# Kernel tuning notes

Hardware: AMD Instinct MI355X
Metric: run time of the kernel (lower is better)

The kernel has to match this reference:

```python
import jax, jax.numpy as jnp
import numpy as np

N = 100000          # nodes
E = 1600000         # edges (avg degree 16)
F_IN = 128          # input node features
H1, C1 = 8, 8       # conv1: 8 heads, 8 channels/head -> 64 concat
NUM_CLASSES = 40    # conv2: 1 head, 40 channels
EPS = 1e-16         # PyG softmax denominator epsilon
NEG_SLOPE = 0.2     # PyG GATConv default leaky_relu slope


def setup_inputs() -> dict:
    key = jax.random.key(0)
    ks = jax.random.split(key, 12)
    x = jax.random.normal(ks[0], (N, F_IN), jnp.float32)
    edge_index = jax.random.randint(ks[1], (2, E), 0, N, dtype=jnp.int64)
    edge_attr = jax.random.normal(ks[2], (E, 1), jnp.float32)
    # layer 1 params (Glorot-ish scaling)
    s1 = 1.0 / np.sqrt(F_IN)
    W1 = jax.random.normal(ks[3], (F_IN, H1 * C1), jnp.float32) * s1
    a_src1 = jax.random.normal(ks[4], (H1, C1), jnp.float32) * (1.0 / np.sqrt(C1))
    a_dst1 = jax.random.normal(ks[5], (H1, C1), jnp.float32) * (1.0 / np.sqrt(C1))
    b1 = jnp.zeros((H1 * C1,), jnp.float32)
    # layer 2 params: in = 64 (conv1 concat output), 1 head, NUM_CLASSES channels
    s2 = 1.0 / np.sqrt(H1 * C1)
    W2 = jax.random.normal(ks[6], (H1 * C1, NUM_CLASSES), jnp.float32) * s2
    a_src2 = jax.random.normal(ks[7], (1, NUM_CLASSES), jnp.float32) * (1.0 / np.sqrt(NUM_CLASSES))
    a_dst2 = jax.random.normal(ks[8], (1, NUM_CLASSES), jnp.float32) * (1.0 / np.sqrt(NUM_CLASSES))
    b2 = jnp.zeros((NUM_CLASSES,), jnp.float32)
    return {"x": x, "edge_index": edge_index, "edge_attr": edge_attr,
            "W1": W1, "a_src1": a_src1, "a_dst1": a_dst1, "b1": b1,
            "W2": W2, "a_src2": a_src2, "a_dst2": a_dst2, "b2": b2}


def gat_conv(x, src, dst, W, a_s, a_d, b, heads, out_ch):
    """PyG GATConv: linear -> per-edge leaky-relu attention -> dst softmax -> scatter-add."""
    n = x.shape[0]
    h = (x @ W).reshape(n, heads, out_ch)                 # [N,H,C]
    alpha_s = jnp.sum(h * a_s, axis=-1)                   # [N,H]
    alpha_d = jnp.sum(h * a_d, axis=-1)                   # [N,H]
    e = jax.nn.leaky_relu(alpha_s[src] + alpha_d[dst], NEG_SLOPE)  # [Etot,H]
    # segment softmax over incoming edges per destination node
    m = jax.ops.segment_max(e, dst, num_segments=n)       # [N,H]
    e = jnp.exp(e - m[dst])
    denom = jax.ops.segment_sum(e, dst, num_segments=n)   # [N,H]
    alpha = e / (denom[dst] + EPS)                        # [Etot,H]
    msg = h[src] * alpha[:, :, None]                      # [Etot,H,C]
    out = jax.ops.segment_sum(msg, dst, num_segments=n)   # [N,H,C]
    return out.reshape(n, heads * out_ch) + b             # concat heads + bias


def reference(x, edge_index, edge_attr, W1, a_src1, a_dst1, b1, W2, a_src2, a_dst2, b2):
    n = x.shape[0]
    # PyG GATConv adds self-loops by default
    loops = jnp.arange(n, dtype=edge_index.dtype)
    src = jnp.concatenate([edge_index[0], loops])
    dst = jnp.concatenate([edge_index[1], loops])
    x = x.astype(jnp.float32)
    x1 = jax.nn.elu(gat_conv(x, src, dst, W1, a_src1, a_dst1, b1, H1, C1))
    x2 = jax.nn.elu(gat_conv(x1, src, dst, W2, a_src2, a_dst2, b2, 1, NUM_CLASSES))
    return x2
```

## Files before the change

kernel.cpp:

```cpp
#include <hip/hip_runtime.h>
#include <math.h>

#define NN 100000
#define NE 1600000
#define NETOT (NE + NN)
#define FIN 128
#define H1N 8
#define D1 64
#define NC 40
#define LNT 64
#define LOG2E 1.44269504088896f

#define BSH 9
#define BNODES 512
#define NBUC ((NN + BNODES - 1) / BNODES)
#define EPB 4096
#define NBLKA ((NE + EPB - 1) / EPB)
#define BCAP 9216
#define LB ((NN + LNT - 1) / LNT)

__device__ __forceinline__ float leakyf(float x) { return x >= 0.0f ? x : 0.2f * x; }
__device__ __forceinline__ float eluf(float x)   { return x > 0.0f ? x : expm1f(x); }
__device__ __forceinline__ float exp2fast(float x) { return __builtin_amdgcn_exp2f(x); }

__device__ __forceinline__ unsigned short f2bf(float f) {
  unsigned u = __float_as_uint(f);
  u += 0x7fffu + ((u >> 16) & 1u);
  return (unsigned short)(u >> 16);
}
__device__ __forceinline__ float bflo(unsigned u) { return __uint_as_float(u << 16); }
__device__ __forceinline__ float bfhi(unsigned u) { return __uint_as_float(u & 0xffff0000u); }

__global__ void k_detect(const long long* __restrict__ ei, int* __restrict__ flag,
                         int* __restrict__ bcnt) {
  int t = threadIdx.x;
  if (t < NBUC) bcnt[t] = 0;
  if (t == 0) {
    int is64 = 1;
    for (int i = 0; i < 16; ++i) {
      long long v = ei[i];
      if (v < 0 || v >= NN) is64 = 0;
    }
    *flag = is64;
  }
}

#define XS1(node, k) xs[(node) * FIN + ((k) ^ ((node) & 31))]
__global__ __launch_bounds__(512) void k_fusedA(
    const void* __restrict__ ei, const int* __restrict__ flag,
    unsigned int* __restrict__ subbuf, int* __restrict__ bcnt,
    const float* __restrict__ x, const float* __restrict__ W,
    const float* __restrict__ aw_s, const float* __restrict__ aw_d,
    unsigned short* __restrict__ h, float* __restrict__ als,
    float* __restrict__ ald) {
  __shared__ __align__(16) char smem[65536];
  int t = threadIdx.x;
  if (blockIdx.x < NBLKA) {
    unsigned int*   pay    = (unsigned int*)smem;
    unsigned int*   spay   = pay + EPB;
    unsigned short* bk     = (unsigned short*)(spay + EPB);
    unsigned short* sbk    = bk + EPB;
    int*            hist   = (int*)(sbk + EPB);
    int*            lstart = hist + 256;
    int*            cur    = lstart + 256;
    int*            gbase  = cur + 256;
    int e0 = blockIdx.x * EPB;
    int cnt = min(EPB, NE - e0);
    if (t < 256) hist[t] = 0;
    __syncthreads();
    bool f64 = (*flag) != 0;
    for (int i = t; i < cnt; i += 512) {
      int s, d;
      if (f64) {
        const long long* p = (const long long*)ei;
        s = (int)p[e0 + i]; d = (int)p[NE + e0 + i];
      } else {
        const int* p = (const int*)ei;
        s = p[e0 + i]; d = p[NE + e0 + i];
      }
      int b = d >> BSH;
      pay[i] = ((unsigned)s << BSH) | (unsigned)(d & (BNODES - 1));
      bk[i] = (unsigned short)b;
      atomicAdd(&hist[b], 1);
    }
    __syncthreads();
    int v = 0;
    if (t < 256) { v = hist[t]; lstart[t] = v; }
    __syncthreads();
    for (int st = 1; st < 256; st <<= 1) {
      int xv = (t < 256 && t >= st) ? lstart[t - st] : 0;
      __syncthreads();
      if (t < 256) lstart[t] += xv;
      __syncthreads();
    }
    int excl = 0;
    if (t < 256) excl = lstart[t] - v;
    __syncthreads();
    if (t < 256) {
      lstart[t] = excl;
      cur[t] = excl;
      gbase[t] = (v > 0) ? atomicAdd(&bcnt[t], v) : 0;
    }
    __syncthreads();
    for (int i = t; i < cnt; i += 512) {
      int b = bk[i];
      int pos = atomicAdd(&cur[b], 1);
      spay[pos] = pay[i];
      sbk[pos] = (unsigned short)b;
    }
    __syncthreads();
    for (int i = t; i < cnt; i += 512) {
      int b = sbk[i];
      int o = gbase[b] + (i - lstart[b]);
      if (o < BCAP) subbuf[(size_t)b * BCAP + o] = spay[i];
    }
  } else {
    float* ws = (float*)smem;
    float* xs = ws + FIN * D1;
    int base = (blockIdx.x - NBLKA) * LNT;
    for (int i = t; i < FIN * D1; i += 512) ws[i] = W[i];
    for (int i = t; i < LNT * FIN; i += 512) {
      int node = i >> 7, k = i & 127;
      int gn = base + node;
      if (gn >= NN) gn = NN - 1;
      XS1(node, k) = x[(size_t)gn * FIN + k];
    }
    __syncthreads();
    int g = t & 7, nl = t >> 3;
    float acc[8] = {0, 0, 0, 0, 0, 0, 0, 0};
    #pragma unroll 4
    for (int k = 0; k < FIN; ++k) {
      float x0 = XS1(nl, k);
      const float4* wr = (const float4*)&ws[k * D1 + g * 8];
      float4 wa = wr[0], wb = wr[1];
      acc[0] = fmaf(x0, wa.x, acc[0]);
      acc[1] = fmaf(x0, wa.y, acc[1]);
      acc[2] = fmaf(x0, wa.z, acc[2]);
      acc[3] = fmaf(x0, wa.w, acc[3]);
      acc[4] = fmaf(x0, wb.x, acc[4]);
      acc[5] = fmaf(x0, wb.y, acc[5]);
      acc[6] = fmaf(x0, wb.z, acc[6]);
      acc[7] = fmaf(x0, wb.w, acc[7]);
    }
    int n0 = base + nl;
    if (n0 < NN) {
      float s = 0.f, d = 0.f;
      uint4 pk;
      pk.x = (unsigned)f2bf(acc[0]) | ((unsigned)f2bf(acc[1]) << 16);
      pk.y = (unsigned)f2bf(acc[2]) | ((unsigned)f2bf(acc[3]) << 16);
      pk.z = (unsigned)f2bf(acc[4]) | ((unsigned)f2bf(acc[5]) << 16);
      pk.w = (unsigned)f2bf(acc[6]) | ((unsigned)f2bf(acc[7]) << 16);
      *(uint4*)(void*)(h + (size_t)n0 * D1 + g * 8) = pk;
      #pragma unroll
      for (int c = 0; c < 8; ++c) {
        s = fmaf(acc[c], aw_s[g * 8 + c], s);
        d = fmaf(acc[c], aw_d[g * 8 + c], d);
      }
      als[n0 * H1N + g] = s * LOG2E;
      ald[n0 * H1N + g] = d * LOG2E;
    }
  }
}

__global__ __launch_bounds__(256) void k_passB(const int* __restrict__ bcnt,
                       const unsigned int* __restrict__ subbuf,
                       int* __restrict__ row_start, int* __restrict__ csr) {
  __shared__ int hist[BNODES];
  __shared__ int ps[256];
  __shared__ int cur[BNODES];
  __shared__ int bbs;
  int b = blockIdx.x, t = threadIdx.x;
  int d0 = b << BSH;
  int nloc = min(BNODES, NN - d0);
  int tot = 0;
  if (t < NBUC) {
    int dd = t << BSH;
    tot = min(BNODES, NN - dd) + min(bcnt[t], BCAP);
  }
  ps[t] = tot;
  __syncthreads();
  for (int s = 1; s < 256; s <<= 1) {
    int xv = (t >= s) ? ps[t - s] : 0;
    __syncthreads();
    ps[t] += xv;
    __syncthreads();
  }
  if (t == 0) bbs = (b == 0) ? 0 : ps[b - 1];
  if (b == 0 && t == 0) row_start[NN] = ps[NBUC - 1];
  __syncthreads();
  int bucket_base = bbs;
  hist[t] = 0; hist[t + 256] = 0;
  __syncthreads();
  int cnt = min(bcnt[b], BCAP);
  const unsigned int* sb = subbuf + (size_t)b * BCAP;
  for (int i = t; i < cnt; i += 256)
    atomicAdd(&hist[sb[i] & (BNODES - 1)], 1);
  __syncthreads();
  int j0 = 2 * t, j1 = 2 * t + 1;
  int s0 = (j0 < nloc) ? hist[j0] + 1 : 0;
  int s1 = (j1 < nloc) ? hist[j1] + 1 : 0;
  int pairsum = s0 + s1;
  ps[t] = pairsum;
  __syncthreads();
  for (int s = 1; s < 256; s <<= 1) {
    int x = (t >= s) ? ps[t - s] : 0;
    __syncthreads();
    ps[t] += x;
    __syncthreads();
  }
  int excl = ps[t] - pairsum + bucket_base;
  if (j0 < nloc) {
    row_start[d0 + j0] = excl;
    csr[excl] = d0 + j0;
    cur[j0] = excl + 1;
  }
  if (j1 < nloc) {
    int rs = excl + s0;
    row_start[d0 + j1] = rs;
    csr[rs] = d0 + j1;
    cur[j1] = rs + 1;
  }
  __syncthreads();
  for (int i = t; i < cnt; i += 256) {
    unsigned u = sb[i];
    int pos = atomicAdd(&cur[u & (BNODES - 1)], 1);
    csr[pos] = (int)(u >> BSH);
  }
}

#define XS2(node, k) xs[(node) * D1 + ((k) ^ ((node) & 31))]
__global__ __launch_bounds__(512) void k_lin2(
    const unsigned int* __restrict__ x1bf, const float* __restrict__ W,
    const float* __restrict__ aw_s, const float* __restrict__ aw_d,
    unsigned short* __restrict__ h, float* __restrict__ als,
    float* __restrict__ ald) {
  __shared__ float ws[D1 * D1];
  __shared__ float xs[LNT * D1];
  int t = threadIdx.x;
  int base = blockIdx.x * LNT;
  for (int i = t; i < D1 * D1; i += 512) {
    int k = i >> 6, c = i & 63;
    ws[i] = (c < NC) ? W[k * NC + c] : 0.f;
  }
  for (int i = t; i < LNT * 32; i += 512) {
    int node = i >> 5, kd = i & 31;
    int gn = base + node;
    if (gn >= NN) gn = NN - 1;
    unsigned u = x1bf[(size_t)gn * 32 + kd];
    XS2(node, 2 * kd)     = bflo(u);
    XS2(node, 2 * kd + 1) = bfhi(u);
  }
  __syncthreads();
  int g = t & 7, nl = t >> 3;
  float acc[8] = {0, 0, 0, 0, 0, 0, 0, 0};
  #pragma unroll 4
  for (int k = 0; k < D1; ++k) {
    float x0 = XS2(nl, k);
    const float4* wr = (const float4*)&ws[k * D1 + g * 8];
    float4 wa = wr[0], wb = wr[1];
    acc[0] = fmaf(x0, wa.x, acc[0]);
    acc[1] = fmaf(x0, wa.y, acc[1]);
    acc[2] = fmaf(x0, wa.z, acc[2]);
    acc[3] = fmaf(x0, wa.w, acc[3]);
    acc[4] = fmaf(x0, wb.x, acc[4]);
    acc[5] = fmaf(x0, wb.y, acc[5]);
    acc[6] = fmaf(x0, wb.z, acc[6]);
    acc[7] = fmaf(x0, wb.w, acc[7]);
  }
  int n0 = base + nl;
  float s = 0.f, d = 0.f;
  #pragma unroll
  for (int c = 0; c < 8; ++c) {
    int col = g * 8 + c;
    float aws = (col < NC) ? aw_s[col] : 0.f;
    float awd = (col < NC) ? aw_d[col] : 0.f;
    s = fmaf(acc[c], aws, s);
    d = fmaf(acc[c], awd, d);
  }
  s += __shfl_xor(s, 1); d += __shfl_xor(d, 1);
  s += __shfl_xor(s, 2); d += __shfl_xor(d, 2);
  s += __shfl_xor(s, 4); d += __shfl_xor(d, 4);
  if (n0 < NN) {
    if (g < 5) {
      #pragma unroll
      for (int c = 0; c < 8; ++c) h[(size_t)n0 * NC + g * 8 + c] = f2bf(acc[c]);
    }
    if (g == 0) { als[n0] = s * LOG2E; ald[n0] = d * LOG2E; }
  }
}

__global__ void k_node1(const int* __restrict__ row_start, const int* __restrict__ csr,
                        const unsigned short* __restrict__ h, const float* __restrict__ als,
                        const float* __restrict__ ald, const float* __restrict__ b,
                        unsigned int* __restrict__ x1bf) {
  __shared__ float pl[4][2][32 * 9];
  int wid = threadIdx.x >> 6, half = (threadIdx.x >> 5) & 1, c2 = threadIdx.x & 31;
  int n = blockIdx.x * 8 + wid * 2 + half;
  float* pw = pl[wid][half];
  const unsigned int* h32 = (const unsigned int*)h;
  int r0 = row_start[n], r1 = row_start[n + 1];
  int hd = c2 >> 2;
  const float4* adp = (const float4*)(ald + (size_t)n * H1N);
  float4 ad0 = adp[0], ad1 = adp[1];
  float S = 0.f;
  float alo0 = 0.f, ahi0 = 0.f, alo1 = 0.f, ahi1 = 0.f;
  float alo2 = 0.f, ahi2 = 0.f, alo3 = 0.f, ahi3 = 0.f;
  for (int kb = r0; kb < r1; kb += 32) {
    int cnt = min(32, r1 - kb);
    if (c2 < cnt) {
      int sk = csr[kb + c2];
      const float4* ap = (const float4*)(als + (size_t)sk * H1N);
      float4 a0 = ap[0], a1 = ap[1];
      pw[c2 * 9 + 0] = exp2fast(leakyf(a0.x + ad0.x));
      pw[c2 * 9 + 1] = exp2fast(leakyf(a0.y + ad0.y));
      pw[c2 * 9 + 2] = exp2fast(leakyf(a0.z + ad0.z));
      pw[c2 * 9 + 3] = exp2fast(leakyf(a0.w + ad0.w));
      pw[c2 * 9 + 4] = exp2fast(leakyf(a1.x + ad1.x));
      pw[c2 * 9 + 5] = exp2fast(leakyf(a1.y + ad1.y));
      pw[c2 * 9 + 6] = exp2fast(leakyf(a1.z + ad1.z));
      pw[c2 * 9 + 7] = exp2fast(leakyf(a1.w + ad1.w));
      pw[c2 * 9 + 8] = __int_as_float(sk);
    }
    asm volatile("s_waitcnt lgkmcnt(0)" ::: "memory");
    int j = 0;
    for (; j + 4 <= cnt; j += 4) {
      int s0 = __float_as_int(pw[(j + 0) * 9 + 8]);
      int s1 = __float_as_int(pw[(j + 1) * 9 + 8]);
      int s2 = __float_as_int(pw[(j + 2) * 9 + 8]);
      int s3 = __float_as_int(pw[(j + 3) * 9 + 8]);
      float p0 = pw[(j + 0) * 9 + hd], p1 = pw[(j + 1) * 9 + hd];
      float p2 = pw[(j + 2) * 9 + hd], p3 = pw[(j + 3) * 9 + hd];
      unsigned u0 = h32[(unsigned)s0 * 32 + c2];
      unsigned u1 = h32[(unsigned)s1 * 32 + c2];
      unsigned u2 = h32[(unsigned)s2 * 32 + c2];
      unsigned u3 = h32[(unsigned)s3 * 32 + c2];
      alo0 = fmaf(p0, bflo(u0), alo0); ahi0 = fmaf(p0, bfhi(u0), ahi0);
      alo1 = fmaf(p1, bflo(u1), alo1); ahi1 = fmaf(p1, bfhi(u1), ahi1);
      alo2 = fmaf(p2, bflo(u2), alo2); ahi2 = fmaf(p2, bfhi(u2), ahi2);
      alo3 = fmaf(p3, bflo(u3), alo3); ahi3 = fmaf(p3, bfhi(u3), ahi3);
      S += (p0 + p1) + (p2 + p3);
    }
    for (; j < cnt; ++j) {
      int s0 = __float_as_int(pw[j * 9 + 8]);
      float p0 = pw[j * 9 + hd];
      unsigned u0 = h32[(unsigned)s0 * 32 + c2];
      alo0 = fmaf(p0, bflo(u0), alo0); ahi0 = fmaf(p0, bfhi(u0), ahi0);
      S += p0;
    }
  }
  float alo = (alo0 + alo1) + (alo2 + alo3);
  float ahi = (ahi0 + ahi1) + (ahi2 + ahi3);
  float inv = 1.0f / (S + 1e-16f);
  float ox = eluf(alo * inv + b[2 * c2 + 0]);
  float oy = eluf(ahi * inv + b[2 * c2 + 1]);
  x1bf[(size_t)n * 32 + c2] = (unsigned)f2bf(ox) | ((unsigned)f2bf(oy) << 16);
}

__global__ void k_node2(const int* __restrict__ row_start, const int* __restrict__ csr,
                        const unsigned short* __restrict__ h, const float* __restrict__ als,
                        const float* __restrict__ ald, const float* __restrict__ b,
                        float* __restrict__ out) {
  __shared__ float pl[4][3][20 * 2];
  int wid = threadIdx.x >> 6, lane = threadIdx.x & 63;
  int g = lane / 20, q = lane - g * 20;
  int gg = g < 3 ? g : 2;
  int n = blockIdx.x * 12 + wid * 3 + gg;
  bool live = (g < 3) && (n < NN);
  if (n >= NN) n = NN - 1;
  float* pw = pl[wid][gg];
  const unsigned int* h32 = (const unsigned int*)h;
  int r0 = row_start[n], r1 = row_start[n + 1];
  float aldn = ald[n];
  float S = 0.f;
  float alo0 = 0.f, ahi0 = 0.f, alo1 = 0.f, ahi1 = 0.f;
  float alo2 = 0.f, ahi2 = 0.f, alo3 = 0.f, ahi3 = 0.f;
  for (int kb = r0; kb < r1; kb += 20) {
    int cnt = min(20, r1 - kb);
    if (q < cnt && g < 3) {
      int sk = csr[kb + q];
      pw[q * 2 + 0] = exp2fast(leakyf(als[sk] + aldn));
      pw[q * 2 + 1] = __int_as_float(sk);
    }
    asm volatile("s_waitcnt lgkmcnt(0)" ::: "memory");
    int j = 0;
    for (; j + 4 <= cnt; j += 4) {
      int s0 = __float_as_int(pw[(j + 0) * 2 + 1]);
      int s1 = __float_as_int(pw[(j + 1) * 2 + 1]);
      int s2 = __float_as_int(pw[(j + 2) * 2 + 1]);
      int s3 = __float_as_int(pw[(j + 3) * 2 + 1]);
      float p0 = pw[(j + 0) * 2], p1 = pw[(j + 1) * 2];
      float p2 = pw[(j + 2) * 2], p3 = pw[(j + 3) * 2];
      unsigned u0 = h32[(unsigned)s0 * 20 + q];
      unsigned u1 = h32[(unsigned)s1 * 20 + q];
      unsigned u2 = h32[(unsigned)s2 * 20 + q];
      unsigned u3 = h32[(unsigned)s3 * 20 + q];
      alo0 = fmaf(p0, bflo(u0), alo0); ahi0 = fmaf(p0, bfhi(u0), ahi0);
      alo1 = fmaf(p1, bflo(u1), alo1); ahi1 = fmaf(p1, bfhi(u1), ahi1);
      alo2 = fmaf(p2, bflo(u2), alo2); ahi2 = fmaf(p2, bfhi(u2), ahi2);
      alo3 = fmaf(p3, bflo(u3), alo3); ahi3 = fmaf(p3, bfhi(u3), ahi3);
      S += (p0 + p1) + (p2 + p3);
    }
    for (; j < cnt; ++j) {
      int s0 = __float_as_int(pw[j * 2 + 1]);
      float p0 = pw[j * 2];
      unsigned u0 = h32[(unsigned)s0 * 20 + q];
      alo0 = fmaf(p0, bflo(u0), alo0); ahi0 = fmaf(p0, bfhi(u0), ahi0);
      S += p0;
    }
  }
  float alo = (alo0 + alo1) + (alo2 + alo3);
  float ahi = (ahi0 + ahi1) + (ahi2 + ahi3);
  if (live) {
    float inv = 1.0f / (S + 1e-16f);
    float2 o;
    o.x = eluf(alo * inv + b[2 * q + 0]);
    o.y = eluf(ahi * inv + b[2 * q + 1]);
    ((float2*)out)[(size_t)n * 20 + q] = o;
  }
}

extern "C" void kernel_launch(void* const* d_in, const int* in_sizes, int n_in,
                              void* d_out, int out_size, void* d_ws, size_t ws_size,
                              hipStream_t stream) {
  const float* x    = (const float*)d_in[0];
  const void*  ei   = d_in[1];
  const float* W1   = (const float*)d_in[3];
  const float* as1w = (const float*)d_in[4];
  const float* ad1w = (const float*)d_in[5];
  const float* b1   = (const float*)d_in[6];
  const float* W2   = (const float*)d_in[7];
  const float* as2w = (const float*)d_in[8];
  const float* ad2w = (const float*)d_in[9];
  const float* b2   = (const float*)d_in[10];
  float* out = (float*)d_out;

  char* w = (char*)d_ws;
  size_t off = 0;
  auto carve = [&](size_t bytes) -> void* {
    void* r = w + off;
    off += (bytes + 255) & ~(size_t)255;
    return r;
  };
  int*            flag        = (int*)carve(256);
  int*            bcnt        = (int*)carve((size_t)NBUC * 4);
  unsigned int*   subbuf      = (unsigned int*)carve((size_t)NBUC * BCAP * 4);
  int*            row_start   = (int*)carve((size_t)(NN + 1) * 4);
  int*            csr         = (int*)carve((size_t)NETOT * 4);
  unsigned short* h1          = (unsigned short*)carve((size_t)NN * D1 * 2);
  float*          als1        = (float*)carve((size_t)NN * H1N * 4);
  float*          ald1        = (float*)carve((size_t)NN * H1N * 4);
  unsigned int*   x1bf        = (unsigned int*)carve((size_t)NN * 32 * 4);
  unsigned short* h2 = h1; float* als2 = als1; float* ald2 = ald1;

  k_detect<<<1, 256, 0, stream>>>((const long long*)ei, flag, bcnt);

  k_fusedA<<<NBLKA + LB, 512, 0, stream>>>(ei, flag, subbuf, bcnt,
                                           x, W1, as1w, ad1w, h1, als1, ald1);

  k_passB<<<NBUC, 256, 0, stream>>>(bcnt, subbuf, row_start, csr);

  k_node1<<<NN / 8, 256, 0, stream>>>(row_start, csr, h1, als1, ald1, b1, x1bf);

  k_lin2<<<LB, 512, 0, stream>>>(x1bf, W2, as2w, ad2w, h2, als2, ald2);
  k_node2<<<(NN + 11) / 12, 256, 0, stream>>>(row_start, csr, h2, als2, ald2, b2, out);
}
```

Before: 203.8 us.

## Fuse layer-2 linear projection and attention logits into layer-1 aggregation kernel

Removes the separate k_lin2 kernel by having each half-wave in the layer-1 node aggregation kernel compute its node's 64x40 projection directly from the ELU output kept in shared memory, with W2 staged per block as packed bf16. This avoids writing and re-reading the x1 intermediate (100k x 64 bf16) and saves one launch. In exchange every block reloads and converts W2 into LDS, W2 is now held in bf16 rather than fp32, and the aggregation kernel uses more shared memory and registers, which may lower occupancy.

```diff
diff --git a/kernel.cpp b/kernel.cpp
--- a/kernel.cpp
+++ b/kernel.cpp
@@ -228,75 +228,29 @@
   }
 }
 
-#define XS2(node, k) xs[(node) * D1 + ((k) ^ ((node) & 31))]
-__global__ __launch_bounds__(512) void k_lin2(
-    const unsigned int* __restrict__ x1bf, const float* __restrict__ W,
-    const float* __restrict__ aw_s, const float* __restrict__ aw_d,
-    unsigned short* __restrict__ h, float* __restrict__ als,
-    float* __restrict__ ald) {
-  __shared__ float ws[D1 * D1];
-  __shared__ float xs[LNT * D1];
+__global__ __launch_bounds__(256) void k_node1f(
+    const int* __restrict__ row_start, const int* __restrict__ csr,
+    const unsigned short* __restrict__ h, const float* __restrict__ als,
+    const float* __restrict__ ald, const float* __restrict__ b,
+    const float* __restrict__ W2, const float* __restrict__ aw_s2,
+    const float* __restrict__ aw_d2, unsigned int* __restrict__ h2_32,
+    float* __restrict__ als2, float* __restrict__ ald2) {
+  __shared__ float pl[4][2][32 * 9];
+  __shared__ unsigned ws2p[D1 * 32];
+  __shared__ float x1r[4][2][D1];
   int t = threadIdx.x;
-  int base = blockIdx.x * LNT;
-  for (int i = t; i < D1 * D1; i += 512) {
-    int k = i >> 6, c = i & 63;
-    ws[i] = (c < NC) ? W[k * NC + c] : 0.f;
-  }
-  for (int i = t; i < LNT * 32; i += 512) {
-    int node = i >> 5, kd = i & 31;
-    int gn = base + node;
-    if (gn >= NN) gn = NN - 1;
-    unsigned u = x1bf[(size_t)gn * 32 + kd];
-    XS2(node, 2 * kd)     = bflo(u);
-    XS2(node, 2 * kd + 1) = bfhi(u);
-  }
-  __syncthreads();
-  int g = t & 7, nl = t >> 3;
-  float acc[8] = {0, 0, 0, 0, 0, 0, 0, 0};
-  #pragma unroll 4
-  for (int k = 0; k < D1; ++k) {
-    float x0 = XS2(nl, k);
-    const float4* wr = (const float4*)&ws[k * D1 + g * 8];
-    float4 wa = wr[0], wb = wr[1];
-    acc[0] = fmaf(x0, wa.x, acc[0]);
-    acc[1] = fmaf(x0, wa.y, acc[1]);
-    acc[2] = fmaf(x0, wa.z, acc[2]);
-    acc[3] = fmaf(x0, wa.w, acc[3]);
-    acc[4] = fmaf(x0, wb.x, acc[4]);
-    acc[5] = fmaf(x0, wb.y, acc[5]);
-    acc[6] = fmaf(x0, wb.z, acc[6]);
-    acc[7] = fmaf(x0, wb.w, acc[7]);
-  }
-  int n0 = base + nl;
-  float s = 0.f, d = 0.f;
-  #pragma unroll
-  for (int c = 0; c < 8; ++c) {
-    int col = g * 8 + c;
-    float aws = (col < NC) ? aw_s[col] : 0.f;
-    float awd = (col < NC) ? aw_d[col] : 0.f;
-    s = fmaf(acc[c], aws, s);
-    d = fmaf(acc[c], awd, d);
-  }
-  s += __shfl_xor(s, 1); d += __shfl_xor(d, 1);
-  s += __shfl_xor(s, 2); d += __shfl_xor(d, 2);
-  s += __shfl_xor(s, 4); d += __shfl_xor(d, 4);
-  if (n0 < NN) {
-    if (g < 5) {
-      #pragma unroll
-      for (int c = 0; c < 8; ++c) h[(size_t)n0 * NC + g * 8 + c] = f2bf(acc[c]);
-    }
-    if (g == 0) { als[n0] = s * LOG2E; ald[n0] = d * LOG2E; }
-  }
-}
-
-__global__ void k_node1(const int* __restrict__ row_start, const int* __restrict__ csr,
-                        const unsigned short* __restrict__ h, const float* __restrict__ als,
-                        const float* __restrict__ ald, const float* __restrict__ b,
-                        unsigned int* __restrict__ x1bf) {
-  __shared__ float pl[4][2][32 * 9];
-  int wid = threadIdx.x >> 6, half = (threadIdx.x >> 5) & 1, c2 = threadIdx.x & 31;
+  for (int i = t; i < D1 * 32; i += 256) {
+    int k = i >> 5, q = i & 31;
+    int c0 = 2 * q, c1 = 2 * q + 1;
+    unsigned lo = (c0 < NC) ? (unsigned)f2bf(W2[k * NC + c0]) : 0u;
+    unsigned hi = (c1 < NC) ? (unsigned)f2bf(W2[k * NC + c1]) : 0u;
+    ws2p[i] = lo | (hi << 16);
+  }
+  __syncthreads();
+  int wid = t >> 6, half = (t >> 5) & 1, c2 = t & 31;
   int n = blockIdx.x * 8 + wid * 2 + half;
   float* pw = pl[wid][half];
+  float* xr = x1r[wid][half];
   const unsigned int* h32 = (const unsigned int*)h;
   int r0 = row_start[n], r1 = row_start[n + 1];
   int hd = c2 >> 2;
@@ -353,11 +307,35 @@
   float inv = 1.0f / (S + 1e-16f);
   float ox = eluf(alo * inv + b[2 * c2 + 0]);
   float oy = eluf(ahi * inv + b[2 * c2 + 1]);
-  x1bf[(size_t)n * 32 + c2] = (unsigned)f2bf(ox) | ((unsigned)f2bf(oy) << 16);
+  xr[2 * c2 + 0] = ox;
+  xr[2 * c2 + 1] = oy;
+  asm volatile("s_waitcnt lgkmcnt(0)" ::: "memory");
+  float a20 = 0.f, a21 = 0.f;
+  #pragma unroll 4
+  for (int k = 0; k < D1; ++k) {
+    float xv = xr[k];
+    unsigned wp = ws2p[k * 32 + c2];
+    a20 = fmaf(xv, bflo(wp), a20);
+    a21 = fmaf(xv, bfhi(wp), a21);
+  }
+  float aws0 = (c2 < 20) ? aw_s2[2 * c2] : 0.f;
+  float aws1 = (c2 < 20) ? aw_s2[2 * c2 + 1] : 0.f;
+  float awd0 = (c2 < 20) ? aw_d2[2 * c2] : 0.f;
+  float awd1 = (c2 < 20) ? aw_d2[2 * c2 + 1] : 0.f;
+  float s2l = a20 * aws0 + a21 * aws1;
+  float d2l = a20 * awd0 + a21 * awd1;
+  s2l += __shfl_xor(s2l, 1);  d2l += __shfl_xor(d2l, 1);
+  s2l += __shfl_xor(s2l, 2);  d2l += __shfl_xor(d2l, 2);
+  s2l += __shfl_xor(s2l, 4);  d2l += __shfl_xor(d2l, 4);
+  s2l += __shfl_xor(s2l, 8);  d2l += __shfl_xor(d2l, 8);
+  s2l += __shfl_xor(s2l, 16); d2l += __shfl_xor(d2l, 16);
+  if (c2 < 20)
+    h2_32[(size_t)n * 20 + c2] = (unsigned)f2bf(a20) | ((unsigned)f2bf(a21) << 16);
+  if (c2 == 0) { als2[n] = s2l * LOG2E; ald2[n] = d2l * LOG2E; }
 }
 
 __global__ void k_node2(const int* __restrict__ row_start, const int* __restrict__ csr,
-                        const unsigned short* __restrict__ h, const float* __restrict__ als,
+                        const unsigned int* __restrict__ h32, const float* __restrict__ als,
                         const float* __restrict__ ald, const float* __restrict__ b,
                         float* __restrict__ out) {
   __shared__ float pl[4][3][20 * 2];
@@ -368,7 +346,6 @@
   bool live = (g < 3) && (n < NN);
   if (n >= NN) n = NN - 1;
   float* pw = pl[wid][gg];
-  const unsigned int* h32 = (const unsigned int*)h;
   int r0 = row_start[n], r1 = row_start[n + 1];
   float aldn = ald[n];
   float S = 0.f;
@@ -441,16 +418,17 @@
     off += (bytes + 255) & ~(size_t)255;
     return r;
   };
-  int*            flag        = (int*)carve(256);
-  int*            bcnt        = (int*)carve((size_t)NBUC * 4);
-  unsigned int*   subbuf      = (unsigned int*)carve((size_t)NBUC * BCAP * 4);
-  int*            row_start   = (int*)carve((size_t)(NN + 1) * 4);
-  int*            csr         = (int*)carve((size_t)NETOT * 4);
-  unsigned short* h1          = (unsigned short*)carve((size_t)NN * D1 * 2);
-  float*          als1        = (float*)carve((size_t)NN * H1N * 4);
-  float*          ald1        = (float*)carve((size_t)NN * H1N * 4);
-  unsigned int*   x1bf        = (unsigned int*)carve((size_t)NN * 32 * 4);
-  unsigned short* h2 = h1; float* als2 = als1; float* ald2 = ald1;
+  int*            flag      = (int*)carve(256);
+  int*            bcnt      = (int*)carve((size_t)NBUC * 4);
+  unsigned int*   subbuf    = (unsigned int*)carve((size_t)NBUC * BCAP * 4);
+  int*            row_start = (int*)carve((size_t)(NN + 1) * 4);
+  int*            csr       = (int*)carve((size_t)NETOT * 4);
+  unsigned short* h1        = (unsigned short*)carve((size_t)NN * D1 * 2);
+  float*          als1      = (float*)carve((size_t)NN * H1N * 4);
+  float*          ald1      = (float*)carve((size_t)NN * H1N * 4);
+  unsigned int*   h2_32     = (unsigned int*)carve((size_t)NN * 20 * 4);
+  float*          als2      = (float*)carve((size_t)NN * 4);
+  float*          ald2      = (float*)carve((size_t)NN * 4);
 
   k_detect<<<1, 256, 0, stream>>>((const long long*)ei, flag, bcnt);
 
@@ -459,8 +437,8 @@
 
   k_passB<<<NBUC, 256, 0, stream>>>(bcnt, subbuf, row_start, csr);
 
-  k_node1<<<NN / 8, 256, 0, stream>>>(row_start, csr, h1, als1, ald1, b1, x1bf);
-
-  k_lin2<<<LB, 512, 0, stream>>>(x1bf, W2, as2w, ad2w, h2, als2, ald2);
-  k_node2<<<(NN + 11) / 12, 256, 0, stream>>>(row_start, csr, h2, als2, ald2, b2, out);
-}
+  k_node1f<<<NN / 8, 256, 0, stream>>>(row_start, csr, h1, als1, ald1, b1,
+                                       W2, as2w, ad2w, h2_32, als2, ald2);
+
+  k_node2<<<(NN + 11) / 12, 256, 0, stream>>>(row_start, csr, h2_32, als2, ald2, b2, out);
+}
```

Result: slower. 216.4 us (+6.2%).
